# Optimization experiments

Hardware: AMD Instinct MI355X
Metric: run time of the kernel (lower is better)

The kernel has to match this reference:

```python
import jax, jax.numpy as jnp
import numpy as np

P_SIZE = 13
B_THRESH = 1.3  # |u| >= b -> hard 1.0
N_POW = 64      # u^n / (u^n + 1)


def make_dct_weight(p):
    idx = np.arange(p)
    Ci = np.where(idx == 0, 1.0 / np.sqrt(2.0), 1.0)
    cos = np.cos((2 * idx[:, None] + 1) * idx[None, :] * np.pi / (2 * p)) * Ci[None, :]  # [x,i]
    P = (2.0 / p) * np.einsum('xi,yj->xyij', cos, cos).reshape(p * p, p * p)
    return P.T.astype(np.float32).reshape(p * p, 1, p, p)


def conv2d(x, w, padding):
    return jax.lax.conv_general_dilated(x, w, (1, 1), padding,
                                        dimension_numbers=('NCHW', 'OIHW', 'NCHW'))


def udiff(u):
    # x^64/(x^64+1), saturated to 1 for |x| >= 1.3 (even power, sign-safe)
    au = jnp.abs(u)
    us = jnp.where(au < B_THRESH, u, 0.0)  # avoid overflow in pow
    y = us ** N_POW
    return jnp.where(au >= B_THRESH, jnp.ones_like(u), y / (y + 1.0))


def setup_inputs() -> dict:
    key = jax.random.key(0)
    k1, _ = jax.random.split(key)
    x = jax.random.uniform(k1, (2, 1, 512, 512), dtype=jnp.float32)
    sigma = jnp.full((1,), 0.1, dtype=jnp.float32)
    W_dct = jnp.asarray(make_dct_weight(P_SIZE))  # [p^2, 1, p, p], learnable in original
    return {"x": x, "sigma": sigma, "W_dct": W_dct}


def reference(x, sigma, W_dct):
    N, _, H, W = x.shape
    p = W_dct.shape[-1]
    pp = p * p
    # patch DCT: [N, p^2, H-p+1, W-p+1]
    t = conv2d(x, W_dct, 'VALID')
    nz = udiff(t / (3.0 * sigma))
    y = t * nz
    w = 1.0 / (1.0 + jnp.sum(nz, axis=1, keepdims=True))  # [N,1,H',W']
    # inverse transform as 1x1 conv with inv(dct matrix)
    Minv = jnp.linalg.inv(W_dct.reshape(pp, pp))
    z = jnp.einsum('kc,nchw->nkhw', Minv, y)
    z = w * z
    # overlap-add fold == conv with spatially-flipped identity patch kernel, full padding
    fold_k = jnp.flip(jnp.eye(pp, dtype=x.dtype).reshape(pp, p, p), axis=(1, 2))[None]  # [1,p^2,p,p]
    folded = conv2d(z, fold_k, [(p - 1, p - 1), (p - 1, p - 1)])  # [N,1,H,W]
    out = folded[:, :, p - 1:H - (p - 1), p - 1:W - (p - 1)]
    divisor = conv2d(w, jnp.ones((1, 1, p, p), x.dtype), 'VALID')
    return out / divisor
```

## Files before the change

kernel.cpp:

```cpp
#include <hip/hip_runtime.h>
#include <math.h>


#define P13    13
#define IMGW   512
#define OUTW   488
#define SEGH   25
#define NSEG   20
#define HCOLS  512
#define HPITCH 16

struct C1mat { float v[P13 * P13]; };

constexpr double kPI = 3.14159265358979323846264338327950288;

constexpr double ccos_pm_pi(double th) {
    double term = 1.0, s = 1.0;
    const double th2 = th * th;
    for (int n = 1; n <= 25; ++n) {
        term *= -th2 / (double)((2 * n - 1) * (2 * n));
        s += term;
    }
    return s;
}
constexpr double csqrt(double v) {
    double x = (v > 1.0) ? v : 1.0;
    for (int i = 0; i < 64; ++i) x = 0.5 * (x + v / x);
    return x;
}
constexpr C1mat make_c1() {
    C1mat m{};
    const double s213 = csqrt(2.0 / 13.0);
    const double is2  = 1.0 / csqrt(2.0);
    for (int x = 0; x < P13; ++x)
        for (int k = 0; k < P13; ++k) {
            int mm = ((2 * x + 1) * k) % 52;
            double th = (mm <= 26) ? (mm * kPI / 26.0) : ((mm - 52) * kPI / 26.0);
            double Ci = (k == 0) ? is2 : 1.0;
            m.v[x * P13 + k] = (float)(s213 * Ci * ccos_pm_pi(th));
        }
    return m;
}
__device__ constexpr C1mat c1c = make_c1();

struct CTab { int idx[P13][P13]; bool neg[P13][P13]; float a[14]; float b[6]; };
constexpr CTab make_ctab() {
    CTab t{};
    const double s213 = csqrt(2.0 / 13.0);
    for (int q = 0; q <= 12; ++q) t.a[q] = (float)(s213 * ccos_pm_pi(q * kPI / 26.0));
    t.a[13] = (float)(s213 / csqrt(2.0));
    for (int q = 0; q < 6; ++q) t.b[q] = (float)(2.0 * ccos_pm_pi((q + 1) * kPI / 13.0));
    for (int r = 0; r < P13; ++r)
        for (int c = 0; c < P13; ++c) {
            if (c == 0) { t.idx[r][c] = 13; t.neg[r][c] = false; continue; }
            int m = ((2 * r + 1) * c) % 52;
            int q; bool n;
            if (m <= 13)      { q = m;      n = false; }
            else if (m <= 26) { q = 26 - m; n = true;  }
            else if (m <= 39) { q = m - 26; n = true;  }
            else              { q = 52 - m; n = false; }
            t.idx[r][c] = q; t.neg[r][c] = n;
        }
    return t;
}
constexpr CTab ctab = make_ctab();

#define KC(r, c) (ctab.neg[(r)][(c)] ? -As[ctab.idx[(r)][(c)]] : As[ctab.idx[(r)][(c)]])

struct FalseT { static constexpr bool value = false; };
struct TrueT  { static constexpr bool value = true; };

#define ROR16_ADD(v, N)                                                        \
    v += __int_as_float(__builtin_amdgcn_mov_dpp(__float_as_int(v),            \
                                                 0x120 + (N), 0xF, 0xF, true))

__device__ __forceinline__ void fold_vert(const float (&tn)[P13], const float (&As)[14],
                                          float w1, float (&H)[P13])
{
#pragma unroll
    for (int dx = 0; dx < 6; ++dx) {
        float E = KC(dx, 0) * tn[0];
#pragma unroll
        for (int i = 2; i < P13; i += 2) E = fmaf(KC(dx, i), tn[i], E);
        float O = KC(dx, 1) * tn[1];
#pragma unroll
        for (int i = 3; i < P13; i += 2) O = fmaf(KC(dx, i), tn[i], O);
        H[dx]      = fmaf(w1, E + O, H[dx]);
        H[12 - dx] = fmaf(w1, E - O, H[12 - dx]);
    }
    float z6 = KC(6, 0) * tn[0];
#pragma unroll
    for (int i = 2; i < P13; i += 2) z6 = fmaf(KC(6, i), tn[i], z6);
    H[6] = fmaf(w1, z6, H[6]);
}

__global__ __launch_bounds__(256) void dct2net_k2(
    const float* __restrict__ xg, const float* __restrict__ sigmag,
    float* __restrict__ Hg, float* __restrict__ Wg)
{
    __shared__ float c1lds[169];
    __shared__ float xlds[4][4][16];
    const int tid = threadIdx.x;
    if (tid < 169) c1lds[tid] = c1c.v[tid];
    __syncthreads();

    const int lane = tid & 63;
    const int wv   = tid >> 6;
    const int g    = lane >> 4;
    const int jj   = lane & 15;
    const int img  = blockIdx.z;
    const int hs   = blockIdx.y * SEGH;
    const int segrows = (OUTW - hs < SEGH) ? (OUTW - hs) : SEGH;
    const int cbw  = blockIdx.x * 16 + wv * 4;
    const int col  = cbw + g;

    const float inv3s = 1.0f / (3.0f * sigmag[0]);
    const float* xin  = xg + (size_t)img * IMGW * IMGW;

    float As[14], Bs[6];
#pragma unroll
    for (int q = 0; q < 14; ++q) As[q] = ctab.a[q];
#pragma unroll
    for (int q = 0; q < 6; ++q) Bs[q] = ctab.b[q];
#pragma unroll
    for (int q = 0; q < 14; ++q) asm("" : "+s"(As[q]));
#pragma unroll
    for (int q = 0; q < 6; ++q) asm("" : "+s"(Bs[q]));

    float c1x[16];
#pragma unroll
    for (int p = 0; p < 16; ++p) {
        int y = p - g;
        int yc = (y < 0) ? 0 : ((y > 12) ? 12 : y);
        int jc = (jj < 13) ? jj : 0;
        float v = c1lds[yc * 13 + jc];
        c1x[p] = (y >= 0 && y < 13 && jj < 13) ? v * inv3s : 0.0f;
    }

    float T0[P13], T1[P13], dr[P13], Hr[P13], wr[12], Rv[P13];
#pragma unroll
    for (int k = 0; k < P13; ++k) { T0[k]=0; T1[k]=0; dr[k]=0; Hr[k]=0; Rv[k]=0; }
#pragma unroll
    for (int k = 0; k < 12; ++k) wr[k] = 0.0f;
    float vs = 0.0f, Rprev = 0.0f;

    int xcol = cbw + (lane & 15); xcol = (xcol < IMGW - 1) ? xcol : (IMGW - 1);
    const float* xlast = xin + (size_t)(IMGW - 1) * IMGW;

    float xq[16];
    float xvA, xvB;
    {
        const float* r0 = xin + (size_t)hs * IMGW;
        xlds[wv][g][jj] = r0[xcol];
        float4 q0 = *(const float4*)&xlds[wv][g][0];
        float4 q1 = *(const float4*)&xlds[wv][g][4];
        float4 q2 = *(const float4*)&xlds[wv][g][8];
        float4 q3 = *(const float4*)&xlds[wv][g][12];
        xq[0]=q0.x; xq[1]=q0.y; xq[2]=q0.z; xq[3]=q0.w;
        xq[4]=q1.x; xq[5]=q1.y; xq[6]=q1.z; xq[7]=q1.w;
        xq[8]=q2.x; xq[9]=q2.y; xq[10]=q2.z; xq[11]=q2.w;
        xq[12]=q3.x; xq[13]=q3.y; xq[14]=q3.z; xq[15]=q3.w;
        const float* r1 = xin + (size_t)(hs + 1) * IMGW;
        xvA = r1[xcol];
    }
    const float* xp = xin + (size_t)(hs + 2) * IMGW;

    float* Hp = Hg + ((size_t)img * OUTW + hs) * HPITCH * HCOLS;
    float* Wp = Wg + ((size_t)img * IMGW + hs) * IMGW;
    const int voH = jj * HCOLS + col;
    const int voW = col;

    auto hdct = [&]() -> float {
        float a0 = c1x[0] * xq[0], a1 = c1x[1] * xq[1];
#pragma unroll
        for (int p = 2; p < 16; p += 2) a0 = fmaf(c1x[p], xq[p], a0);
#pragma unroll
        for (int p = 3; p < 16; p += 2) a1 = fmaf(c1x[p], xq[p], a1);
        return a0 + a1;
    };
    auto advance = [&](float xvW, float& xvL) {
        xlds[wv][g][jj] = xvW;
        float4 q0 = *(const float4*)&xlds[wv][g][0];
        float4 q1 = *(const float4*)&xlds[wv][g][4];
        float4 q2 = *(const float4*)&xlds[wv][g][8];
        float4 q3 = *(const float4*)&xlds[wv][g][12];
        xq[0]=q0.x; xq[1]=q0.y; xq[2]=q0.z; xq[3]=q0.w;
        xq[4]=q1.x; xq[5]=q1.y; xq[6]=q1.z; xq[7]=q1.w;
        xq[8]=q2.x; xq[9]=q2.y; xq[10]=q2.z; xq[11]=q2.w;
        xq[12]=q3.x; xq[13]=q3.y; xq[14]=q3.z; xq[15]=q3.w;
        const float* xr = (xp < xlast) ? xp : xlast;
        xvL = xr[xcol]; xp += IMGW;
    };
    auto pushRv = [&](float Rn) {
#pragma unroll
        for (int q = 0; q < P13 - 1; ++q) Rv[q] = Rv[q + 1];
        Rv[P13 - 1] = Rn;
    };
    auto pushd = [&](float Rn) {
        float dn = Rn - Rprev; Rprev = Rn;
#pragma unroll
        for (int q = 0; q < P13 - 1; ++q) dr[q] = dr[q + 1];
        dr[P13 - 1] = dn;
    };
    auto matvec = [&](float (&T)[P13]) {
        float Se[6], So[6];
#pragma unroll
        for (int k = 0; k < 6; ++k) { Se[k] = Rv[k] + Rv[12 - k]; So[k] = Rv[k] - Rv[12 - k]; }
#pragma unroll
        for (int i = 0; i < P13; ++i) {
            float t;
            if ((i & 1) == 0) {
                t = KC(6, i) * Rv[6];
#pragma unroll
                for (int k = 0; k < 6; ++k) t = fmaf(KC(k, i), Se[k], t);
            } else {
                t = KC(0, i) * So[0];
#pragma unroll
                for (int k = 1; k < 6; ++k) t = fmaf(KC(k, i), So[k], t);
            }
            T[i] = t;
        }
    };
    auto sf = [&](const float (&T)[P13], bool rt) {
        float tn[P13];
        float pz0 = 0.0f, pz1 = 0.0f, pz2 = 0.0f, pz3 = 0.0f;
#pragma unroll
        for (int i = 0; i < P13; ++i) {
            float p2 = fminf(T[i] * T[i], 1.69f);
            float p4 = p2 * p2, p8 = p4 * p4, p16 = p8 * p8, p32 = p16 * p16, p64 = p32 * p32;
            float r  = __builtin_amdgcn_rcpf(p64 + 1.0f);
            if ((i & 3) == 0) pz0 += r;
            else if ((i & 3) == 1) pz1 += r;
            else if ((i & 3) == 2) pz2 += r;
            else pz3 += r;
            tn[i] = fmaf(-T[i], r, T[i]);
        }
        float pnz = 13.0f - ((pz0 + pz1) + (pz2 + pz3));
        ROR16_ADD(pnz, 1); ROR16_ADD(pnz, 2); ROR16_ADD(pnz, 4); ROR16_ADD(pnz, 8);
        const float w = __builtin_amdgcn_rcpf(1.0f + pnz);
        vs += w;
        fold_vert(tn, As, w, Hr);
        if (rt) {
            if (jj < 13) Hp[voH] = Hr[0];
            Hp += HPITCH * HCOLS;
            if (jj == 0) Wp[voW] = vs;
            Wp += IMGW;
            vs -= wr[0];
        }
#pragma unroll
        for (int q = 0; q < 11; ++q) wr[q] = wr[q + 1];
        wr[11] = w;
#pragma unroll
        for (int q = 0; q < P13 - 1; ++q) Hr[q] = Hr[q + 1];
        Hr[P13 - 1] = 0.0f;
    };
    auto recur = [&](auto INTOT0, float& xvW, float& xvL, bool rt) {
        float Rn = hdct();
        advance(xvW, xvL);
        float dn = Rn - Rprev; Rprev = Rn;
        float dl = dr[0];
#pragma unroll
        for (int q = 0; q < P13 - 1; ++q) dr[q] = dr[q + 1];
        dr[P13 - 1] = dn;
        float Pe = dn - dl, Po = dn + dl;
#pragma unroll
        for (int i = 0; i < P13; ++i) {
            float tp2 = decltype(INTOT0)::value ? T0[i] : T1[i];
            float tp1 = decltype(INTOT0)::value ? T1[i] : T0[i];
            float c2 = (i == 0) ? 2.0f : ((i <= 6) ? Bs[i - 1] : -Bs[12 - i]);
            float t = fmaf(c2, tp1, -tp2);
            float kc = (i == 0) ? As[13] : As[i];
            t = (i & 1) ? fmaf(-kc, Po, t) : fmaf(kc, Pe, t);
            if constexpr (decltype(INTOT0)::value) T0[i] = t; else T1[i] = t;
        }
        if constexpr (decltype(INTOT0)::value) sf(T0, rt); else sf(T1, rt);
    };

    { float Rn = hdct(); advance(xvA, xvB); Rprev = Rn; pushRv(Rn); }
    { float Rn = hdct(); advance(xvB, xvA); pushd(Rn); pushRv(Rn); }
#pragma unroll 1
    for (int k = 2; k < 12; k += 2) {
        float Rn = hdct(); advance(xvA, xvB); pushd(Rn); pushRv(Rn);
        float Rm = hdct(); advance(xvB, xvA); pushd(Rm); pushRv(Rm);
    }
    { float Rn = hdct(); advance(xvA, xvB); pushd(Rn); pushRv(Rn); matvec(T0); sf(T0, false); }
    { float Rn = hdct(); advance(xvB, xvA); pushd(Rn); pushRv(Rn); matvec(T1); sf(T1, false); }
    {
        int ks = 0; const int S = 10 + segrows;
#pragma unroll 1
        while (ks + 2 <= S) {
            recur(TrueT{},  xvA, xvB, ks     >= 10);
            recur(FalseT{}, xvB, xvA, ks + 1 >= 10);
            ks += 2;
        }
        if (ks < S) recur(TrueT{}, xvA, xvB, ks >= 10);
    }
}

__global__ __launch_bounds__(64) void dct2net_k3(
    const float* __restrict__ Hg, const float* __restrict__ Wg,
    const float* __restrict__ sigmag, float* __restrict__ outg)
{
    __shared__ float U[76][15];
    __shared__ float vw[80];
    const int lane = threadIdx.x;
    const int img  = blockIdx.z;
    const int a    = blockIdx.y;
    const int cb   = blockIdx.x * 64;

    const float t3s = 3.0f * sigmag[0];

    float As[14];
#pragma unroll
    for (int q = 0; q < 14; ++q) As[q] = ctab.a[q];
#pragma unroll
    for (int q = 0; q < 14; ++q) asm("" : "+s"(As[q]));

    int c = cb + lane; c = (c < 499) ? c : 499;
    const float* hb = Hg + ((size_t)img * OUTW + a) * HPITCH * HCOLS + c;
    float hv[P13];
#pragma unroll
    for (int j = 0; j < P13; ++j) hv[j] = hb[j * HCOLS];
    float wm = Wg[((size_t)img * IMGW + a) * IMGW + c];

    const bool halo = (lane < 12);
    float sv[P13]; float ws = 0.0f;
#pragma unroll
    for (int j = 0; j < P13; ++j) sv[j] = 0.0f;
    if (halo) {
        int c2 = cb + 64 + lane; c2 = (c2 < 499) ? c2 : 499;
        const float* hq = Hg + ((size_t)img * OUTW + a) * HPITCH * HCOLS + c2;
#pragma unroll
        for (int j = 0; j < P13; ++j) sv[j] = hq[j * HCOLS];
        ws = Wg[((size_t)img * IMGW + a) * IMGW + c2];
    }

    auto buildU = [&](const float (&h)[P13], int uli) {
#pragma unroll
        for (int dy = 0; dy < 6; ++dy) {
            float e = KC(dy, 0) * h[0];
#pragma unroll
            for (int j = 2; j < P13; j += 2) e = fmaf(KC(dy, j), h[j], e);
            float o = KC(dy, 1) * h[1];
#pragma unroll
            for (int j = 3; j < P13; j += 2) o = fmaf(KC(dy, j), h[j], o);
            U[uli][dy]      = e + o;
            U[uli][12 - dy] = e - o;
        }
        float gsum = ((h[4] - h[2]) + (h[8] - h[6])) + (h[12] - h[10]);
        U[uli][6] = fmaf(As[0], gsum, As[13] * h[0]);
    };

    buildU(hv, lane);
    vw[lane] = wm;
    if (halo) {
        buildU(sv, 64 + lane);
        vw[64 + lane] = ws;
    }

    float num = 0.0f;
#pragma unroll
    for (int dy = 0; dy < P13; ++dy) num += U[lane + 12 - dy][dy];
    float den = 0.0f;
#pragma unroll
    for (int d = 0; d < P13; ++d) den += vw[lane + d];
    const int ow = cb + lane;
    if (ow < OUTW)
        outg[((size_t)img * OUTW + a) * OUTW + ow] =
            num * t3s * __builtin_amdgcn_rcpf(den);
}

extern "C" void kernel_launch(void* const* d_in, const int* in_sizes, int n_in,
                              void* d_out, int out_size, void* d_ws, size_t ws_size,
                              hipStream_t stream)
{
    const float* x     = (const float*)d_in[0];
    const float* sigma = (const float*)d_in[1];
    float* out = (float*)d_out;

    float* Hg = (float*)d_ws;
    float* Wg = Hg + (size_t)2 * OUTW * HPITCH * HCOLS;

    dct2net_k2<<<dim3(32, NSEG, 2), 256, 0, stream>>>(x, sigma, Hg, Wg);
    dct2net_k3<<<dim3(8, 488, 2), 64, 0, stream>>>(Hg, Wg, sigma, out);
}
```

Measured before the change: 184.3 us.

## Move delay lines to LDS rings and halve Hr shifting; enlarge segments

The per-thread shift registers for the column-difference history and the weight history are replaced by ring buffers in shared memory, read one step ahead to hide LDS latency. The Hr accumulator now uses a two-phase rotated index, so it shifts once every two rows instead of every row. The segment height grows from 25 to 31 rows, which cuts the number of segments and the per-segment warm-up recurrence. This is meant to lower register pressure and shift moves, at the cost of LDS traffic, fewer blocks, and more serial rows per block.

```diff
diff --git a/kernel.cpp b/kernel.cpp
--- a/kernel.cpp
+++ b/kernel.cpp
@@ -5,8 +5,8 @@
 #define P13    13
 #define IMGW   512
 #define OUTW   488
-#define SEGH   25
-#define NSEG   20
+#define SEGH   31
+#define NSEG   16
 #define HCOLS  512
 #define HPITCH 16
 
@@ -74,6 +74,7 @@
     v += __int_as_float(__builtin_amdgcn_mov_dpp(__float_as_int(v),            \
                                                  0x120 + (N), 0xF, 0xF, true))
 
+template<int R>
 __device__ __forceinline__ void fold_vert(const float (&tn)[P13], const float (&As)[14],
                                           float w1, float (&H)[P13])
 {
@@ -85,13 +86,13 @@
         float O = KC(dx, 1) * tn[1];
 #pragma unroll
         for (int i = 3; i < P13; i += 2) O = fmaf(KC(dx, i), tn[i], O);
-        H[dx]      = fmaf(w1, E + O, H[dx]);
-        H[12 - dx] = fmaf(w1, E - O, H[12 - dx]);
+        H[(dx + R) % P13]      = fmaf(w1, E + O, H[(dx + R) % P13]);
+        H[(12 - dx + R) % P13] = fmaf(w1, E - O, H[(12 - dx + R) % P13]);
     }
     float z6 = KC(6, 0) * tn[0];
 #pragma unroll
     for (int i = 2; i < P13; i += 2) z6 = fmaf(KC(6, i), tn[i], z6);
-    H[6] = fmaf(w1, z6, H[6]);
+    H[(6 + R) % P13] = fmaf(w1, z6, H[(6 + R) % P13]);
 }
 
 __global__ __launch_bounds__(256) void dct2net_k2(
@@ -100,6 +101,8 @@
 {
     __shared__ float c1lds[169];
     __shared__ float xlds[4][4][16];
+    __shared__ float dline[13][256];
+    __shared__ float wline[12][256];
     const int tid = threadIdx.x;
     if (tid < 169) c1lds[tid] = c1c.v[tid];
     __syncthreads();
@@ -137,12 +140,12 @@
         c1x[p] = (y >= 0 && y < 13 && jj < 13) ? v * inv3s : 0.0f;
     }
 
-    float T0[P13], T1[P13], dr[P13], Hr[P13], wr[12], Rv[P13];
-#pragma unroll
-    for (int k = 0; k < P13; ++k) { T0[k]=0; T1[k]=0; dr[k]=0; Hr[k]=0; Rv[k]=0; }
-#pragma unroll
-    for (int k = 0; k < 12; ++k) wr[k] = 0.0f;
+    float T0[P13], T1[P13], Hr[P13], Rv[P13];
+#pragma unroll
+    for (int k = 0; k < P13; ++k) { T0[k]=0; T1[k]=0; Hr[k]=0; Rv[k]=0; }
     float vs = 0.0f, Rprev = 0.0f;
+    float dl_pre = 0.0f, wold_pre = 0.0f;
+    int dslot = 0, wslot = 0;
 
     int xcol = cbw + (lane & 15); xcol = (xcol < IMGW - 1) ? xcol : (IMGW - 1);
     const float* xlast = xin + (size_t)(IMGW - 1) * IMGW;
@@ -191,16 +194,18 @@
         const float* xr = (xp < xlast) ? xp : xlast;
         xvL = xr[xcol]; xp += IMGW;
     };
+    auto dring = [&](float dn) -> float {
+        float dl = dl_pre;
+        dline[dslot][tid] = dn;
+        const int dn1 = (dslot == 12) ? 0 : dslot + 1;
+        dl_pre = dline[dn1][tid];
+        dslot = dn1;
+        return dl;
+    };
     auto pushRv = [&](float Rn) {
 #pragma unroll
         for (int q = 0; q < P13 - 1; ++q) Rv[q] = Rv[q + 1];
         Rv[P13 - 1] = Rn;
-    };
-    auto pushd = [&](float Rn) {
-        float dn = Rn - Rprev; Rprev = Rn;
-#pragma unroll
-        for (int q = 0; q < P13 - 1; ++q) dr[q] = dr[q + 1];
-        dr[P13 - 1] = dn;
     };
     auto matvec = [&](float (&T)[P13]) {
         float Se[6], So[6];
@@ -221,7 +226,8 @@
             T[i] = t;
         }
     };
-    auto sf = [&](const float (&T)[P13], bool rt) {
+    auto sf = [&](auto PH, const float (&T)[P13], bool rt) {
+        constexpr int R = decltype(PH)::value ? 1 : 0;
         float tn[P13];
         float pz0 = 0.0f, pz1 = 0.0f, pz2 = 0.0f, pz3 = 0.0f;
 #pragma unroll
@@ -239,29 +245,26 @@
         ROR16_ADD(pnz, 1); ROR16_ADD(pnz, 2); ROR16_ADD(pnz, 4); ROR16_ADD(pnz, 8);
         const float w = __builtin_amdgcn_rcpf(1.0f + pnz);
         vs += w;
-        fold_vert(tn, As, w, Hr);
+        fold_vert<R>(tn, As, w, Hr);
+        float wold = wold_pre;
+        wline[wslot][tid] = w;
+        const int wn1 = (wslot == 11) ? 0 : wslot + 1;
+        wold_pre = wline[wn1][tid];
+        wslot = wn1;
         if (rt) {
-            if (jj < 13) Hp[voH] = Hr[0];
+            if (jj < 13) Hp[voH] = Hr[R];
             Hp += HPITCH * HCOLS;
             if (jj == 0) Wp[voW] = vs;
             Wp += IMGW;
-            vs -= wr[0];
-        }
-#pragma unroll
-        for (int q = 0; q < 11; ++q) wr[q] = wr[q + 1];
-        wr[11] = w;
-#pragma unroll
-        for (int q = 0; q < P13 - 1; ++q) Hr[q] = Hr[q + 1];
-        Hr[P13 - 1] = 0.0f;
-    };
-    auto recur = [&](auto INTOT0, float& xvW, float& xvL, bool rt) {
+            vs -= wold;
+        }
+        Hr[R] = 0.0f;
+    };
+    auto recur = [&](auto INTOT0, auto PH, float& xvW, float& xvL, bool rt) {
         float Rn = hdct();
         advance(xvW, xvL);
         float dn = Rn - Rprev; Rprev = Rn;
-        float dl = dr[0];
-#pragma unroll
-        for (int q = 0; q < P13 - 1; ++q) dr[q] = dr[q + 1];
-        dr[P13 - 1] = dn;
+        float dl = dring(dn);
         float Pe = dn - dl, Po = dn + dl;
 #pragma unroll
         for (int i = 0; i < P13; ++i) {
@@ -273,27 +276,37 @@
             t = (i & 1) ? fmaf(-kc, Po, t) : fmaf(kc, Pe, t);
             if constexpr (decltype(INTOT0)::value) T0[i] = t; else T1[i] = t;
         }
-        if constexpr (decltype(INTOT0)::value) sf(T0, rt); else sf(T1, rt);
+        if constexpr (decltype(INTOT0)::value) sf(PH, T0, rt); else sf(PH, T1, rt);
+    };
+    auto shift2 = [&]() {
+        float h0 = Hr[0];
+#pragma unroll
+        for (int q = 0; q < 11; ++q) Hr[q] = Hr[q + 2];
+        Hr[11] = h0; Hr[12] = 0.0f;
     };
 
     { float Rn = hdct(); advance(xvA, xvB); Rprev = Rn; pushRv(Rn); }
-    { float Rn = hdct(); advance(xvB, xvA); pushd(Rn); pushRv(Rn); }
+    { float Rn = hdct(); advance(xvB, xvA); dring(Rn - Rprev); Rprev = Rn; pushRv(Rn); }
 #pragma unroll 1
     for (int k = 2; k < 12; k += 2) {
-        float Rn = hdct(); advance(xvA, xvB); pushd(Rn); pushRv(Rn);
-        float Rm = hdct(); advance(xvB, xvA); pushd(Rm); pushRv(Rm);
-    }
-    { float Rn = hdct(); advance(xvA, xvB); pushd(Rn); pushRv(Rn); matvec(T0); sf(T0, false); }
-    { float Rn = hdct(); advance(xvB, xvA); pushd(Rn); pushRv(Rn); matvec(T1); sf(T1, false); }
+        { float Rn = hdct(); advance(xvA, xvB); dring(Rn - Rprev); Rprev = Rn; pushRv(Rn); }
+        { float Rn = hdct(); advance(xvB, xvA); dring(Rn - Rprev); Rprev = Rn; pushRv(Rn); }
+    }
+    { float Rn = hdct(); advance(xvA, xvB); dring(Rn - Rprev); Rprev = Rn; pushRv(Rn);
+      matvec(T0); sf(FalseT{}, T0, false); }
+    { float Rn = hdct(); advance(xvB, xvA); dring(Rn - Rprev); Rprev = Rn; pushRv(Rn);
+      matvec(T1); sf(TrueT{}, T1, false); }
+    shift2();
     {
         int ks = 0; const int S = 10 + segrows;
 #pragma unroll 1
         while (ks + 2 <= S) {
-            recur(TrueT{},  xvA, xvB, ks     >= 10);
-            recur(FalseT{}, xvB, xvA, ks + 1 >= 10);
+            recur(TrueT{},  FalseT{}, xvA, xvB, ks     >= 10);
+            recur(FalseT{}, TrueT{},  xvB, xvA, ks + 1 >= 10);
+            shift2();
             ks += 2;
         }
-        if (ks < S) recur(TrueT{}, xvA, xvB, ks >= 10);
+        if (ks < S) recur(TrueT{}, FalseT{}, xvA, xvB, ks >= 10);
     }
 }
 
```

After: 175.5 us. -4.8%, faster.

## Software-pipeline row loads and output stores; enlarge segment height

Applied to the files above, without the earlier changes.

Issues the next-row global load at the start of each recurrence step and defers the previous step's H/W output stores into the next iteration, so memory latency overlaps with the DCT arithmetic. The LDS staging of the new row now happens after the compute instead of in the middle. Segment height goes from 25 to 31 rows with 16 segments, which means fewer blocks and less warm-up overhead per output row, but also less parallelism. The deferred store needs a final flush after the loop.

```diff
diff --git a/kernel.cpp b/kernel.cpp
--- a/kernel.cpp
+++ b/kernel.cpp
@@ -5,8 +5,8 @@
 #define P13    13
 #define IMGW   512
 #define OUTW   488
-#define SEGH   25
-#define NSEG   20
+#define SEGH   31
+#define NSEG   16
 #define HCOLS  512
 #define HPITCH 16
 
@@ -143,6 +143,7 @@
 #pragma unroll
     for (int k = 0; k < 12; ++k) wr[k] = 0.0f;
     float vs = 0.0f, Rprev = 0.0f;
+    float Hout = 0.0f, Wout = 0.0f;
 
     int xcol = cbw + (lane & 15); xcol = (xcol < IMGW - 1) ? xcol : (IMGW - 1);
     const float* xlast = xin + (size_t)(IMGW - 1) * IMGW;
@@ -170,6 +171,16 @@
     const int voH = jj * HCOLS + col;
     const int voW = col;
 
+    auto loadNext = [&](float& xvL) {
+        const float* xr = (xp < xlast) ? xp : xlast;
+        xvL = xr[xcol]; xp += IMGW;
+    };
+    auto storeOut = [&]() {
+        if (jj < 13) Hp[voH] = Hout;
+        Hp += HPITCH * HCOLS;
+        if (jj == 0) Wp[voW] = Wout;
+        Wp += IMGW;
+    };
     auto hdct = [&]() -> float {
         float a0 = c1x[0] * xq[0], a1 = c1x[1] * xq[1];
 #pragma unroll
@@ -178,7 +189,7 @@
         for (int p = 3; p < 16; p += 2) a1 = fmaf(c1x[p], xq[p], a1);
         return a0 + a1;
     };
-    auto advance = [&](float xvW, float& xvL) {
+    auto stage = [&](float xvW) {
         xlds[wv][g][jj] = xvW;
         float4 q0 = *(const float4*)&xlds[wv][g][0];
         float4 q1 = *(const float4*)&xlds[wv][g][4];
@@ -188,8 +199,6 @@
         xq[4]=q1.x; xq[5]=q1.y; xq[6]=q1.z; xq[7]=q1.w;
         xq[8]=q2.x; xq[9]=q2.y; xq[10]=q2.z; xq[11]=q2.w;
         xq[12]=q3.x; xq[13]=q3.y; xq[14]=q3.z; xq[15]=q3.w;
-        const float* xr = (xp < xlast) ? xp : xlast;
-        xvL = xr[xcol]; xp += IMGW;
     };
     auto pushRv = [&](float Rn) {
 #pragma unroll
@@ -221,7 +230,7 @@
             T[i] = t;
         }
     };
-    auto sf = [&](const float (&T)[P13], bool rt) {
+    auto sf = [&](const float (&T)[P13], bool retireNow) {
         float tn[P13];
         float pz0 = 0.0f, pz1 = 0.0f, pz2 = 0.0f, pz3 = 0.0f;
 #pragma unroll
@@ -240,12 +249,10 @@
         const float w = __builtin_amdgcn_rcpf(1.0f + pnz);
         vs += w;
         fold_vert(tn, As, w, Hr);
-        if (rt) {
-            if (jj < 13) Hp[voH] = Hr[0];
-            Hp += HPITCH * HCOLS;
-            if (jj == 0) Wp[voW] = vs;
-            Wp += IMGW;
-            vs -= wr[0];
+        if (retireNow) {
+            Hout = Hr[0];
+            Wout = vs;
+            vs  -= wr[0];
         }
 #pragma unroll
         for (int q = 0; q < 11; ++q) wr[q] = wr[q + 1];
@@ -254,9 +261,10 @@
         for (int q = 0; q < P13 - 1; ++q) Hr[q] = Hr[q + 1];
         Hr[P13 - 1] = 0.0f;
     };
-    auto recur = [&](auto INTOT0, float& xvW, float& xvL, bool rt) {
+    auto recur = [&](auto INTOT0, float& xvW, float& xvL, bool storePrev, bool retireNow) {
+        loadNext(xvL);
+        if (storePrev) storeOut();
         float Rn = hdct();
-        advance(xvW, xvL);
         float dn = Rn - Rprev; Rprev = Rn;
         float dl = dr[0];
 #pragma unroll
@@ -273,27 +281,31 @@
             t = (i & 1) ? fmaf(-kc, Po, t) : fmaf(kc, Pe, t);
             if constexpr (decltype(INTOT0)::value) T0[i] = t; else T1[i] = t;
         }
-        if constexpr (decltype(INTOT0)::value) sf(T0, rt); else sf(T1, rt);
-    };
-
-    { float Rn = hdct(); advance(xvA, xvB); Rprev = Rn; pushRv(Rn); }
-    { float Rn = hdct(); advance(xvB, xvA); pushd(Rn); pushRv(Rn); }
+        if constexpr (decltype(INTOT0)::value) sf(T0, retireNow); else sf(T1, retireNow);
+        stage(xvW);
+    };
+
+    { loadNext(xvB); float Rn = hdct(); Rprev = Rn; pushRv(Rn); stage(xvA); }
+    { loadNext(xvA); float Rn = hdct(); pushd(Rn); pushRv(Rn); stage(xvB); }
 #pragma unroll 1
     for (int k = 2; k < 12; k += 2) {
-        float Rn = hdct(); advance(xvA, xvB); pushd(Rn); pushRv(Rn);
-        float Rm = hdct(); advance(xvB, xvA); pushd(Rm); pushRv(Rm);
-    }
-    { float Rn = hdct(); advance(xvA, xvB); pushd(Rn); pushRv(Rn); matvec(T0); sf(T0, false); }
-    { float Rn = hdct(); advance(xvB, xvA); pushd(Rn); pushRv(Rn); matvec(T1); sf(T1, false); }
+        { loadNext(xvB); float Rn = hdct(); pushd(Rn); pushRv(Rn); stage(xvA); }
+        { loadNext(xvA); float Rn = hdct(); pushd(Rn); pushRv(Rn); stage(xvB); }
+    }
+    { loadNext(xvB); float Rn = hdct(); pushd(Rn); pushRv(Rn);
+      matvec(T0); sf(T0, false); stage(xvA); }
+    { loadNext(xvA); float Rn = hdct(); pushd(Rn); pushRv(Rn);
+      matvec(T1); sf(T1, false); stage(xvB); }
     {
         int ks = 0; const int S = 10 + segrows;
 #pragma unroll 1
         while (ks + 2 <= S) {
-            recur(TrueT{},  xvA, xvB, ks     >= 10);
-            recur(FalseT{}, xvB, xvA, ks + 1 >= 10);
+            recur(TrueT{},  xvA, xvB, ks     >= 11, ks     >= 10);
+            recur(FalseT{}, xvB, xvA, ks + 1 >= 11, ks + 1 >= 10);
             ks += 2;
         }
-        if (ks < S) recur(TrueT{}, xvA, xvB, ks >= 10);
+        if (ks < S) recur(TrueT{}, xvA, xvB, ks >= 11, ks >= 10);
+        storeOut();
     }
 }
 
```

Result: faster. 173.6 us (-5.8%).
